# Performance work log

Measured on AMD Instinct MI355X. Metric: run time of the kernel, lower is better.

Reference implementation:

```python
import jax, jax.numpy as jnp
import numpy as np

# NSA hyperparams (match init_kwargs)
D_BLK = 64    # d: block stride
L_CMP = 64    # compression block length (== d -> non-overlapping blocks)
L_SLC = 64    # selection block length (== l_cmp == d -> P_slc = P_cmp)
BQ = 64       # block_size_q
TOPK = 16     # slc_top_k
WL, WR = 512, 0  # sliding window (left, right)


def _nsa_forward(q, k, v, w_k, b_k, w_v, b_v, w_gate, b_gate, seqlen):
    S, qh, dim = q.shape
    kv = k.shape[1]
    H = qh // kv
    b = S // seqlen          # number of equal-length packed sequences
    s = seqlen
    scale = dim ** -0.5
    f32 = jnp.float32

    # [b, s, kv, H, e]: q head g*H+h belongs to kv head g (repeat_interleave layout)
    q5 = q.reshape(b, s, kv, H, dim)
    k3 = k.reshape(b, s, kv, dim)
    v3 = v.reshape(b, s, kv, dim)

    # ---- block compression (extract_blocks + cmp_linear over block length) ----
    n_blk = s // D_BLK
    kb = k.reshape(b, n_blk, D_BLK, kv, dim)
    vb = v.reshape(b, n_blk, D_BLK, kv, dim)
    K_cmp = jnp.einsum('bntke,t->bnke', kb, w_k) + b_k[0]
    V_cmp = jnp.einsum('bntke,t->bnke', vb, w_v) + b_v[0]

    # ---- compressed attention (per sequence, fp32 softmax) ----
    sc = jnp.einsum('bqkhe,bnke->bkhqn', q5, K_cmp).astype(f32) * scale
    P = jax.nn.softmax(sc, axis=-1)
    out_cmp = jnp.einsum('bkhqn,bnke->bqkhe', P.astype(q.dtype), V_cmp)

    # ---- selection scores: pool P over q-blocks and GQA groups, then top-k ----
    nqb = s // BQ
    pooled = P.reshape(b, kv, H, nqb, BQ, n_blk).sum(axis=(2, 4))  # [b,kv,nqb,n_blk]
    idx = jax.lax.top_k(pooled, TOPK)[1]                            # [b,kv,nqb,TOPK]

    # gather selected K/V blocks (shared by all queries in a q-block / GQA group)
    kb2 = jnp.transpose(kb, (0, 3, 1, 2, 4))  # [b,kv,n_blk,l,e]
    vb2 = jnp.transpose(vb, (0, 3, 1, 2, 4))
    gather = jax.vmap(jax.vmap(lambda blocks, i: blocks[i]))
    K_sel = gather(kb2, idx)  # [b,kv,nqb,TOPK,l,e]
    V_sel = gather(vb2, idx)

    # ---- selected-block attention ----
    qblk = q5.reshape(b, nqb, BQ, kv, H, dim)
    sc2 = jnp.einsum('bnckhe,bkntle->bkhnctl', qblk, K_sel).astype(f32) * scale
    sc2 = sc2.reshape(b, kv, H, nqb, BQ, TOPK * L_SLC)
    P2 = jax.nn.softmax(sc2, axis=-1).astype(q.dtype)
    out_slc = jnp.einsum('bkhncm,bknme->bnckhe', P2,
                         V_sel.reshape(b, kv, nqb, TOPK * L_SLC, dim))
    out_slc = out_slc.reshape(b, s, kv, H, dim)

    # ---- sliding-window attention (window_size=(WL, WR), non-causal flag) ----
    sw = jnp.einsum('bikhe,bjke->bkhij', q5, k3).astype(f32) * scale
    i = jnp.arange(s)[:, None]
    j = jnp.arange(s)[None, :]
    valid = (j >= i - WL) & (j <= i + WR)
    sw = jnp.where(valid, sw, -jnp.inf)
    Pw = jax.nn.softmax(sw, axis=-1).astype(q.dtype)
    out_win = jnp.einsum('bkhij,bjke->bikhe', Pw, v3)

    # ---- gated fusion of the three branches ----
    gate = jax.nn.sigmoid(jnp.einsum('bqkhe,ec->bqkhc', q5, w_gate) + b_gate)
    out = (gate[..., 0:1] * out_cmp
           + gate[..., 1:2] * out_slc
           + gate[..., 2:3] * out_win)
    return out.reshape(S, qh, dim)


def setup_inputs() -> dict:
    key = jax.random.key(0)
    ks = jax.random.split(key, 9)
    S, qh, kvh, dim = 4096, 8, 2, 128
    inp = {
        'q': jax.random.normal(ks[0], (S, qh, dim), jnp.float32),
        'k': jax.random.normal(ks[1], (S, kvh, dim), jnp.float32),
        'v': jax.random.normal(ks[2], (S, kvh, dim), jnp.float32),
        'w_k': jax.random.normal(ks[3], (L_CMP,), jnp.float32) * (L_CMP ** -0.5),
        'b_k': jax.random.normal(ks[4], (1,), jnp.float32) * 0.02,
        'w_v': jax.random.normal(ks[5], (L_CMP,), jnp.float32) * (L_CMP ** -0.5),
        'b_v': jax.random.normal(ks[6], (1,), jnp.float32) * 0.02,
        'w_gate': jax.random.normal(ks[7], (dim, 3), jnp.float32) * (dim ** -0.5),
        'b_gate': jax.random.normal(ks[8], (3,), jnp.float32) * 0.02,
        'seqlen': 2048,
    }
    return inp


def reference(q, k, v, w_k, b_k, w_v, b_v, w_gate, b_gate, seqlen):
    return _nsa_forward(q, k, v, w_k, b_k, w_v, b_v, w_gate, b_gate, seqlen)
```

## Files before the change

kernel.cpp:

```cpp
#include <hip/hip_runtime.h>
#include <hip/hip_bf16.h>


#define SEQ   2048
#define NB    2
#define KV    2
#define NH    4
#define QH    8
#define DIM   128
#define NBLK  32
#define NQB   32
#define NTOP  16
#define SCALE 0.08838834764831845f
#define QSC   0.12751831795244785f
#define QS    36
#define RS    144
#define PLS   33
#define VP    72

typedef unsigned short ushort_t;
using bf16x8 = __attribute__((ext_vector_type(8))) short;
using f32x4  = __attribute__((ext_vector_type(4))) float;

__device__ __forceinline__ unsigned pkbf(float a, float b){
  union { __hip_bfloat162 h; unsigned u; } cv;
  cv.h = __float22bfloat162_rn(make_float2(a, b));
  return cv.u;
}

__device__ __forceinline__ void async16(ushort_t* l, const ushort_t* g){
  __builtin_amdgcn_global_load_lds(
      (const __attribute__((address_space(1))) unsigned int*)(size_t)g,
      (__attribute__((address_space(3))) unsigned int*)(size_t)l,
      16, 0, 0);
}

__global__ __launch_bounds__(256) void prep_k(
    const float* __restrict__ k, const float* __restrict__ v,
    const float* __restrict__ w_k, const float* __restrict__ b_k,
    const float* __restrict__ w_v, const float* __restrict__ b_v,
    ushort_t* __restrict__ Kb, ushort_t* __restrict__ VT,
    float* __restrict__ Kc, float* __restrict__ Vc)
{
  int blk = blockIdx.x;
  int db = blk & 1, rb = (blk >> 1) & 31, bbg = blk >> 6;
  int bb = bbg >> 1, g = bbg & 1;
  int tid = threadIdx.x;
  __shared__ ushort_t T[64*VP];
  __shared__ float wks[64], wvs[64];
  __shared__ float accK[16][64], accV[16][64];

  if (tid < 64){ wks[tid] = w_k[tid]; wvs[tid] = w_v[tid]; }
  __syncthreads();

  float4 sk = {0,0,0,0}, sv = {0,0,0,0};
  for (int jj = 0; jj < 4; ++jj){
    int i = tid + jj*256;
    int r = i >> 4, ds = i & 15;
    size_t src = ((size_t)(bb*SEQ + rb*64 + r)*KV + g)*DIM + db*64 + ds*4;
    float4 kx = *(const float4*)(k + src);
    float4 vx = *(const float4*)(v + src);
    uint2 kk; kk.x = pkbf(kx.x,kx.y); kk.y = pkbf(kx.z,kx.w);
    size_t rowb = ((size_t)bbg*SEQ + rb*64 + r)*DIM*2;
    int swz = (db*128 + ds*8) ^ ((r & 7) << 4);
    *(uint2*)((char*)Kb + rowb + swz) = kk;
    unsigned v01 = pkbf(vx.x,vx.y), v23 = pkbf(vx.z,vx.w);
    T[(ds*4+0)*VP + r] = (ushort_t)(v01 & 0xffffu);
    T[(ds*4+1)*VP + r] = (ushort_t)(v01 >> 16);
    T[(ds*4+2)*VP + r] = (ushort_t)(v23 & 0xffffu);
    T[(ds*4+3)*VP + r] = (ushort_t)(v23 >> 16);
    float a = wks[r], b = wvs[r];
    sk.x += a*kx.x; sk.y += a*kx.y; sk.z += a*kx.z; sk.w += a*kx.w;
    sv.x += b*vx.x; sv.y += b*vx.y; sv.z += b*vx.z; sv.w += b*vx.w;
  }
  *(float4*)&accK[tid>>4][(tid&15)*4] = sk;
  *(float4*)&accV[tid>>4][(tid&15)*4] = sv;
  __syncthreads();

  for (int jj = 0; jj < 4; ++jj){
    int i = tid + jj*256;
    int d = i >> 4, seg = i & 15;
    uint2 u = *(uint2*)&T[d*VP + seg*4];
    size_t rowb = ((size_t)bbg*DIM + db*64 + d)*SEQ*2;
    int swz = (seg*8) ^ ((d & 7) << 4);
    *(uint2*)((char*)VT + rowb + rb*128 + swz) = u;
  }

  size_t obase = ((size_t)(bbg*NBLK + rb))*DIM + db*64;
  if (tid < 64){
    float s = 0.f;
#pragma unroll
    for (int i = 0; i < 16; ++i) s += accK[i][tid];
    Kc[obase + tid] = s + b_k[0];
  } else if (tid < 128){
    int d = tid - 64;
    float s = 0.f;
#pragma unroll
    for (int i = 0; i < 16; ++i) s += accV[i][d];
    Vc[obase + d] = s + b_v[0];
  }
}

__global__ __launch_bounds__(256) void cmp_attn_k(
    const float* __restrict__ q, const float* __restrict__ Kc,
    const float* __restrict__ Vc,
    const float* __restrict__ w_gate, const float* __restrict__ b_gate,
    float* __restrict__ pooled_part, float* __restrict__ out)
{
  int blk = blockIdx.x;
  int h  = blk & 3;
  int qb = (blk >> 2) & (NQB-1);
  int g  = (blk >> 7) & 1;
  int bb = blk >> 8;
  int tid = threadIdx.x;
  int qi = tid >> 2, c = tid & 3;

  __shared__ float Ks[32*RS];
  __shared__ float Vs[32*RS];
  __shared__ float Pl[64*PLS];

  const float4* Ksrc = (const float4*)(Kc + (size_t)(bb*KV + g) * NBLK * DIM);
  const float4* Vsrc = (const float4*)(Vc + (size_t)(bb*KV + g) * NBLK * DIM);
  for (int i = tid; i < 1024; i += 256){
    int row = i >> 5, seg = i & 31;
    int dst = row*RS + (seg>>3)*QS + (seg&7)*4;
    ((float4*)(Ks+dst))[0] = Ksrc[i];
    ((float4*)(Vs+dst))[0] = Vsrc[i];
  }
  __syncthreads();

  int row = bb*SEQ + qb*64 + qi;
  const float* qptr = q + ((size_t)row*QH + g*NH + h)*DIM;

  float sc[8];
#pragma unroll
  for (int nn = 0; nn < 8; ++nn) sc[nn] = 0.f;
  float gp = 0.f;
  for (int qq = 0; qq < 4; ++qq){
    float qv[32];
    const float4* q4 = (const float4*)(qptr + qq*32);
#pragma unroll
    for (int j = 0; j < 8; ++j){
      float4 u = q4[j];
      qv[4*j+0]=u.x; qv[4*j+1]=u.y; qv[4*j+2]=u.z; qv[4*j+3]=u.w;
    }
#pragma unroll
    for (int d = 0; d < 32; ++d) gp += qv[d]*w_gate[(qq*32+d)*3 + 0];
#pragma unroll
    for (int nn = 0; nn < 8; ++nn){
      int n = nn*4 + c;
      const float4* kr = (const float4*)(Ks + n*RS + qq*QS);
      float p = 0.f;
#pragma unroll
      for (int j = 0; j < 8; ++j){
        float4 u = kr[j];
        p += qv[4*j+0]*u.x + qv[4*j+1]*u.y + qv[4*j+2]*u.z + qv[4*j+3]*u.w;
      }
      sc[nn] += p;
    }
  }
  float g0 = 1.f/(1.f + expf(-(gp + b_gate[0])));

#pragma unroll
  for (int nn = 0; nn < 8; ++nn) sc[nn] *= SCALE;
  float m = sc[0];
#pragma unroll
  for (int nn = 1; nn < 8; ++nn) m = fmaxf(m, sc[nn]);
  m = fmaxf(m, __shfl_xor(m, 1)); m = fmaxf(m, __shfl_xor(m, 2));
  float l = 0.f;
#pragma unroll
  for (int nn = 0; nn < 8; ++nn){ sc[nn] = expf(sc[nn]-m); l += sc[nn]; }
  l += __shfl_xor(l, 1); l += __shfl_xor(l, 2);
  float inv = 1.f/l;
#pragma unroll
  for (int nn = 0; nn < 8; ++nn) Pl[qi*PLS + nn*4 + c] = sc[nn]*inv;
  __syncthreads();

  if (tid < NBLK){
    float s = 0.f;
    for (int q2 = 0; q2 < 64; ++q2) s += Pl[q2*PLS + tid];
    pooled_part[(size_t)blk*NBLK + tid] = s;
  }

  float o[32];
#pragma unroll
  for (int d = 0; d < 32; ++d) o[d] = 0.f;
  for (int n = 0; n < NBLK; ++n){
    float pb = Pl[qi*PLS + n];
    const float4* vr = (const float4*)(Vs + n*RS + c*QS);
#pragma unroll
    for (int j = 0; j < 8; ++j){
      float4 u = vr[j];
      o[4*j+0] += pb*u.x; o[4*j+1] += pb*u.y;
      o[4*j+2] += pb*u.z; o[4*j+3] += pb*u.w;
    }
  }
  float* op = out + ((size_t)row*QH + g*NH + h)*DIM + c*32;
#pragma unroll
  for (int d = 0; d < 32; ++d) op[d] = g0*o[d];
}

__global__ __launch_bounds__(512, 2) void attn_k(
    const float* __restrict__ q, const ushort_t* __restrict__ Kb,
    const ushort_t* __restrict__ VT, const float* __restrict__ pp,
    const float* __restrict__ w_gate, const float* __restrict__ b_gate,
    float* __restrict__ slcbuf, float* __restrict__ out)
{
  int idx = blockIdx.x;
  int x = idx & 7, low = idx & 1, u = idx >> 3;
  int bbg = x >> 1;
  int j = u*2 + low;
  int role = j >> 5;
  int qb = j & 31;
  int bb = bbg >> 1, g = bbg & 1;

  int tid = threadIdx.x;
  int lane = tid & 63, w = tid >> 6;
  int quad = lane >> 4, l15 = lane & 15;
  int h = w & 3, qh2 = w >> 2;
  int xr = (l15 & 7) << 4;

  __shared__ ushort_t Ks[2][64*128];
  __shared__ ushort_t VTs[2][128*64];
  __shared__ ushort_t Ps[256*VP];
  __shared__ float gbuf[256];
  __shared__ int   idxs[NTOP];

  if (role == 0 && tid < 64){
    int n = lane;
    float val = -INFINITY;
    if (n < NBLK){
      const float* p0 = pp + ((size_t)((bb*KV+g)*NQB + qb)*NH)*NBLK + n;
      val = (p0[0] + p0[NBLK]) + (p0[2*NBLK] + p0[3*NBLK]);
    }
    for (int t = 0; t < NTOP; ++t){
      float bv = val; int bi = n;
      for (int mm = 1; mm < 32; mm <<= 1){
        float ov = __shfl_xor(bv, mm);
        int   oi = __shfl_xor(bi, mm);
        if (ov > bv || (ov == bv && oi < bi)){ bv = ov; bi = oi; }
      }
      if (lane == 0) idxs[t] = bi;
      if (n == bi) val = -INFINITY;
    }
  }

  const float* qrow0 = q + ((size_t)(bb*SEQ + qb*64 + qh2*32 + l15)*QH + g*NH + h)*DIM;
  const float* qrow1 = qrow0 + (size_t)16*QH*DIM;
  int gcol = 1 + role;
  bf16x8 qfrag0[4], qfrag1[4];
  float gp0 = 0.f, gp1 = 0.f;
#pragma unroll
  for (int kc = 0; kc < 4; ++kc){
    int d0 = kc*32 + quad*8;
    float4 a0 = *(const float4*)(qrow0 + d0);
    float4 a1 = *(const float4*)(qrow0 + d0 + 4);
    float4 b0 = *(const float4*)(qrow1 + d0);
    float4 b1 = *(const float4*)(qrow1 + d0 + 4);
    float qa[8] = {a0.x,a0.y,a0.z,a0.w,a1.x,a1.y,a1.z,a1.w};
    float qc[8] = {b0.x,b0.y,b0.z,b0.w,b1.x,b1.y,b1.z,b1.w};
#pragma unroll
    for (int jj = 0; jj < 8; ++jj){
      float wg = w_gate[(d0+jj)*3 + gcol];
      gp0 += qa[jj]*wg; gp1 += qc[jj]*wg;
    }
    union { unsigned uu[4]; bf16x8 v8; } t0, t1;
#pragma unroll
    for (int p2 = 0; p2 < 4; ++p2){
      t0.uu[p2] = pkbf(qa[2*p2]*QSC, qa[2*p2+1]*QSC);
      t1.uu[p2] = pkbf(qc[2*p2]*QSC, qc[2*p2+1]*QSC);
    }
    qfrag0[kc] = t0.v8; qfrag1[kc] = t1.v8;
  }
  gp0 += __shfl_xor(gp0,16); gp0 += __shfl_xor(gp0,32);
  gp1 += __shfl_xor(gp1,16); gp1 += __shfl_xor(gp1,32);
  if (quad == 0){
    gbuf[w*32 + l15]      = 1.f/(1.f + __expf(-(gp0 + b_gate[gcol])));
    gbuf[w*32 + 16 + l15] = 1.f/(1.f + __expf(-(gp1 + b_gate[gcol])));
  }
  __syncthreads();
  float gl0[4], gl1[4];
#pragma unroll
  for (int r = 0; r < 4; ++r){
    gl0[r] = gbuf[w*32 + quad*4 + r];
    gl1[r] = gbuf[w*32 + 16 + quad*4 + r];
  }

  const ushort_t* kbase  = Kb + (size_t)bbg*SEQ*DIM;
  const ushort_t* vtbase = VT + (size_t)bbg*DIM*SEQ;

  int kb0 = (qb >= 8) ? (qb - 8) : 0;
  int nph = (role == 0) ? NTOP : (qb - kb0 + 1);
  int qi0 = qh2*32 + l15, qi1 = qi0 + 16;

  float m10 = -INFINITY, l10 = 0.f, m11 = -INFINITY, l11 = 0.f;
  f32x4 oacc0[8], oacc1[8];
  const f32x4 zero4 = {0.f,0.f,0.f,0.f};
#pragma unroll
  for (int dt = 0; dt < 8; ++dt){ oacc0[dt] = zero4; oacc1[dt] = zero4; }

  auto stage = [&](int bufi, int kb_){
    const ushort_t* ksrc = kbase + (size_t)kb_*64*DIM;
#pragma unroll
    for (int jj = 0; jj < 2; ++jj)
      async16(&Ks[bufi][(jj*512 + w*64)*8], ksrc + (size_t)(tid + jj*512)*8);
    const ushort_t* vsrc = vtbase + kb_*64;
#pragma unroll
    for (int jj = 0; jj < 2; ++jj){
      int i = tid + jj*512;
      int d = i >> 3, sg = i & 7;
      async16(&VTs[bufi][(jj*512 + w*64)*8], vsrc + (size_t)d*SEQ + sg*8);
    }
  };

  stage(0, (role == 0) ? idxs[0] : kb0);

  for (int t = 0; t < nph; ++t){
    int cur = t & 1;
    int kb = (role == 0) ? idxs[t] : (kb0 + t);
    __syncthreads();
    if (t+1 < nph){
      int kbn = (role == 0) ? idxs[t+1] : (kb0 + t + 1);
      stage(cur ^ 1, kbn);
    }
    __builtin_amdgcn_sched_barrier(0);

    f32x4 sacc0[4], sacc1[4];
#pragma unroll
    for (int nt = 0; nt < 4; ++nt){ sacc0[nt] = zero4; sacc1[nt] = zero4; }
    __builtin_amdgcn_s_setprio(1);
#pragma unroll
    for (int kc = 0; kc < 4; ++kc){
#pragma unroll
      for (int nt = 0; nt < 4; ++nt){
        bf16x8 a = *(bf16x8*)((char*)&Ks[cur][0] + (nt*16 + l15)*256
                              + ((kc*64 + quad*16) ^ xr));
        sacc0[nt] = __builtin_amdgcn_mfma_f32_16x16x32_bf16(a, qfrag0[kc], sacc0[nt], 0, 0, 0);
        sacc1[nt] = __builtin_amdgcn_mfma_f32_16x16x32_bf16(a, qfrag1[kc], sacc1[nt], 0, 0, 0);
      }
    }
    __builtin_amdgcn_s_setprio(0);

    bool mlow  = (role == 1) && (kb == qb - 8);
    bool mhigh = (role == 1) && (kb == qb);
    bool domask = mlow | mhigh;

    auto softmax_qt = [&](f32x4* sc, float& m1r, float& l1r, int qi_l,
                          bool& skipped) -> float {
      float mx = -INFINITY;
      if (domask){
#pragma unroll
        for (int nt = 0; nt < 4; ++nt)
#pragma unroll
          for (int r = 0; r < 4; ++r){
            int key = nt*16 + quad*4 + r;
            float sv = sc[nt][r];
            bool valid = (!mlow || key >= qi_l) && (!mhigh || key <= qi_l);
            sv = valid ? sv : -INFINITY;
            sc[nt][r] = sv;
            mx = fmaxf(mx, sv);
          }
      } else {
#pragma unroll
        for (int nt = 0; nt < 4; ++nt)
#pragma unroll
          for (int r = 0; r < 4; ++r) mx = fmaxf(mx, sc[nt][r]);
      }
      mx = fmaxf(mx, __shfl_xor(mx, 16));
      mx = fmaxf(mx, __shfl_xor(mx, 32));
      float al = 1.f;
      skipped = __all(mx <= m1r + 8.f);
      if (!skipped){
        float mn = fmaxf(m1r, mx);
        al = exp2f(m1r - mn);
        m1r = mn;
      }
      float s0 = 0.f;
#pragma unroll
      for (int nt = 0; nt < 4; ++nt)
#pragma unroll
        for (int r = 0; r < 4; ++r){
          float pe = exp2f(sc[nt][r] - m1r);
          sc[nt][r] = pe;
          s0 += pe;
        }
      s0 += __shfl_xor(s0, 16);
      s0 += __shfl_xor(s0, 32);
      l1r = l1r*al + s0;
      return al;
    };
    bool sk0, sk1;
    float al0 = softmax_qt(sacc0, m10, l10, qi0, sk0);
    float al1 = softmax_qt(sacc1, m11, l11, qi1, sk1);

#pragma unroll
    for (int nt = 0; nt < 4; ++nt){
      uint2 p0, p1;
      p0.x = pkbf(sacc0[nt][0], sacc0[nt][1]);
      p0.y = pkbf(sacc0[nt][2], sacc0[nt][3]);
      p1.x = pkbf(sacc1[nt][0], sacc1[nt][1]);
      p1.y = pkbf(sacc1[nt][2], sacc1[nt][3]);
      *(uint2*)&Ps[(w*32 + l15)*VP + nt*16 + quad*4] = p0;
      *(uint2*)&Ps[(w*32 + 16 + l15)*VP + nt*16 + quad*4] = p1;
    }

    if (!sk0){
      float ar[4];
#pragma unroll
      for (int r = 0; r < 4; ++r) ar[r] = __shfl(al0, quad*4 + r);
#pragma unroll
      for (int dt = 0; dt < 8; ++dt)
#pragma unroll
        for (int r = 0; r < 4; ++r) oacc0[dt][r] *= ar[r];
    }
    if (!sk1){
      float ar[4];
#pragma unroll
      for (int r = 0; r < 4; ++r) ar[r] = __shfl(al1, quad*4 + r);
#pragma unroll
      for (int dt = 0; dt < 8; ++dt)
#pragma unroll
        for (int r = 0; r < 4; ++r) oacc1[dt][r] *= ar[r];
    }

#pragma unroll
    for (int kc2 = 0; kc2 < 2; ++kc2){
      bf16x8 pa0 = *(bf16x8*)&Ps[(w*32 + l15)*VP + kc2*32 + quad*8];
      bf16x8 pa1 = *(bf16x8*)&Ps[(w*32 + 16 + l15)*VP + kc2*32 + quad*8];
      __builtin_amdgcn_s_setprio(1);
#pragma unroll
      for (int dt = 0; dt < 8; ++dt){
        bf16x8 vb8 = *(bf16x8*)((char*)&VTs[cur][0] + (dt*16 + l15)*128
                                + ((kc2*64 + quad*16) ^ xr));
        oacc0[dt] = __builtin_amdgcn_mfma_f32_16x16x32_bf16(pa0, vb8, oacc0[dt], 0, 0, 0);
        oacc1[dt] = __builtin_amdgcn_mfma_f32_16x16x32_bf16(pa1, vb8, oacc1[dt], 0, 0, 0);
      }
      __builtin_amdgcn_s_setprio(0);
    }
  }

  float lr0[4], lr1[4];
#pragma unroll
  for (int r = 0; r < 4; ++r){
    lr0[r] = __shfl(l10, quad*4 + r);
    lr1[r] = __shfl(l11, quad*4 + r);
  }
#pragma unroll
  for (int r = 0; r < 4; ++r){
    float s20 = gl0[r] / lr0[r];
    float s21 = gl1[r] / lr1[r];
    size_t ob0 = ((size_t)(bb*SEQ + qb*64 + qh2*32 + quad*4 + r)*QH + g*NH + h)*DIM + l15;
    size_t ob1 = ob0 + (size_t)16*QH*DIM;
    if (role == 0){
      float* op0 = slcbuf + ob0;
      float* op1 = slcbuf + ob1;
#pragma unroll
      for (int dt = 0; dt < 8; ++dt){
        op0[dt*16] = s20 * oacc0[dt][r];
        op1[dt*16] = s21 * oacc1[dt][r];
      }
    } else {
      float* op0 = out + ob0;
      float* op1 = out + ob1;
#pragma unroll
      for (int dt = 0; dt < 8; ++dt){
        op0[dt*16] += s20 * oacc0[dt][r];
        op1[dt*16] += s21 * oacc1[dt][r];
      }
    }
  }
}

__global__ __launch_bounds__(256) void merge_k(const float* __restrict__ slcbuf,
                                               float* __restrict__ out){
  int i = blockIdx.x * 256 + threadIdx.x;
  float4 a = ((const float4*)slcbuf)[i];
  float4 b = ((float4*)out)[i];
  b.x += a.x; b.y += a.y; b.z += a.z; b.w += a.w;
  ((float4*)out)[i] = b;
}

extern "C" void kernel_launch(void* const* d_in, const int* in_sizes, int n_in,
                              void* d_out, int out_size, void* d_ws, size_t ws_size,
                              hipStream_t stream) {
  const float* q      = (const float*)d_in[0];
  const float* k      = (const float*)d_in[1];
  const float* v      = (const float*)d_in[2];
  const float* w_k    = (const float*)d_in[3];
  const float* b_k    = (const float*)d_in[4];
  const float* w_v    = (const float*)d_in[5];
  const float* b_v    = (const float*)d_in[6];
  const float* w_gate = (const float*)d_in[7];
  const float* b_gate = (const float*)d_in[8];
  float* out = (float*)d_out;

  float* ws     = (float*)d_ws;
  float* Kc     = ws;
  float* Vc     = ws + 16384;
  float* pp     = ws + 32768;
  float* slcbuf = ws + 49152;
  ushort_t* Kb  = (ushort_t*)(ws + 4243456);
  ushort_t* VT  = Kb + 1048576;

  prep_k    <<<256, 256, 0, stream>>>(k, v, w_k, b_k, w_v, b_v, Kb, VT, Kc, Vc);
  cmp_attn_k<<<NB*KV*NQB*NH, 256, 0, stream>>>(q, Kc, Vc, w_gate, b_gate, pp, out);
  attn_k    <<<256, 512, 0, stream>>>(q, Kb, VT, pp, w_gate, b_gate, slcbuf, out);
  merge_k   <<<4096, 256, 0, stream>>>(slcbuf, out);
}
```

Before: 178.6 us.

## Fuse compressed attention into selection kernel using split-bf16 MFMA

Removes the separate fp32 compressed-attention kernel and computes compressed scores, softmax, pooled selection scores and the compressed output inside the role-0 blocks of the main attention kernel. The products use MFMA with hi/lo bf16 splitting of Q, compressed K, V and P to keep close to fp32 accuracy, and top-k now reads pooled scores from shared memory instead of a global partial buffer. Role-1 blocks now write out directly rather than accumulating into it. This saves a kernel launch and the global traffic for pooled partials and the compressed output. In exchange, role-0 blocks carry extra serial work and more shared memory, which may reduce occupancy.

New measurement: 166.3 us. -6.8%, faster.

```diff
diff --git a/kernel.cpp b/kernel.cpp
--- a/kernel.cpp
+++ b/kernel.cpp
@@ -13,10 +13,8 @@
 #define NTOP  16
 #define SCALE 0.08838834764831845f
 #define QSC   0.12751831795244785f
-#define QS    36
-#define RS    144
-#define PLS   33
 #define VP    72
+#define VCS   40
 
 typedef unsigned short ushort_t;
 using bf16x8 = __attribute__((ext_vector_type(8))) short;
@@ -26,6 +24,15 @@
   union { __hip_bfloat162 h; unsigned u; } cv;
   cv.h = __float22bfloat162_rn(make_float2(a, b));
   return cv.u;
+}
+__device__ __forceinline__ ushort_t b16(float f){
+  union { float f; unsigned i; } x; x.f = f;
+  unsigned r = x.i + 0x7fffu + ((x.i >> 16) & 1u);
+  return (ushort_t)(r >> 16);
+}
+__device__ __forceinline__ float fb(ushort_t h){
+  union { unsigned i; float f; } x; x.i = ((unsigned)h) << 16;
+  return x.f;
 }
 
 __device__ __forceinline__ void async16(ushort_t* l, const ushort_t* g){
@@ -101,108 +108,10 @@
   }
 }
 
-__global__ __launch_bounds__(256) void cmp_attn_k(
-    const float* __restrict__ q, const float* __restrict__ Kc,
-    const float* __restrict__ Vc,
-    const float* __restrict__ w_gate, const float* __restrict__ b_gate,
-    float* __restrict__ pooled_part, float* __restrict__ out)
-{
-  int blk = blockIdx.x;
-  int h  = blk & 3;
-  int qb = (blk >> 2) & (NQB-1);
-  int g  = (blk >> 7) & 1;
-  int bb = blk >> 8;
-  int tid = threadIdx.x;
-  int qi = tid >> 2, c = tid & 3;
-
-  __shared__ float Ks[32*RS];
-  __shared__ float Vs[32*RS];
-  __shared__ float Pl[64*PLS];
-
-  const float4* Ksrc = (const float4*)(Kc + (size_t)(bb*KV + g) * NBLK * DIM);
-  const float4* Vsrc = (const float4*)(Vc + (size_t)(bb*KV + g) * NBLK * DIM);
-  for (int i = tid; i < 1024; i += 256){
-    int row = i >> 5, seg = i & 31;
-    int dst = row*RS + (seg>>3)*QS + (seg&7)*4;
-    ((float4*)(Ks+dst))[0] = Ksrc[i];
-    ((float4*)(Vs+dst))[0] = Vsrc[i];
-  }
-  __syncthreads();
-
-  int row = bb*SEQ + qb*64 + qi;
-  const float* qptr = q + ((size_t)row*QH + g*NH + h)*DIM;
-
-  float sc[8];
-#pragma unroll
-  for (int nn = 0; nn < 8; ++nn) sc[nn] = 0.f;
-  float gp = 0.f;
-  for (int qq = 0; qq < 4; ++qq){
-    float qv[32];
-    const float4* q4 = (const float4*)(qptr + qq*32);
-#pragma unroll
-    for (int j = 0; j < 8; ++j){
-      float4 u = q4[j];
-      qv[4*j+0]=u.x; qv[4*j+1]=u.y; qv[4*j+2]=u.z; qv[4*j+3]=u.w;
-    }
-#pragma unroll
-    for (int d = 0; d < 32; ++d) gp += qv[d]*w_gate[(qq*32+d)*3 + 0];
-#pragma unroll
-    for (int nn = 0; nn < 8; ++nn){
-      int n = nn*4 + c;
-      const float4* kr = (const float4*)(Ks + n*RS + qq*QS);
-      float p = 0.f;
-#pragma unroll
-      for (int j = 0; j < 8; ++j){
-        float4 u = kr[j];
-        p += qv[4*j+0]*u.x + qv[4*j+1]*u.y + qv[4*j+2]*u.z + qv[4*j+3]*u.w;
-      }
-      sc[nn] += p;
-    }
-  }
-  float g0 = 1.f/(1.f + expf(-(gp + b_gate[0])));
-
-#pragma unroll
-  for (int nn = 0; nn < 8; ++nn) sc[nn] *= SCALE;
-  float m = sc[0];
-#pragma unroll
-  for (int nn = 1; nn < 8; ++nn) m = fmaxf(m, sc[nn]);
-  m = fmaxf(m, __shfl_xor(m, 1)); m = fmaxf(m, __shfl_xor(m, 2));
-  float l = 0.f;
-#pragma unroll
-  for (int nn = 0; nn < 8; ++nn){ sc[nn] = expf(sc[nn]-m); l += sc[nn]; }
-  l += __shfl_xor(l, 1); l += __shfl_xor(l, 2);
-  float inv = 1.f/l;
-#pragma unroll
-  for (int nn = 0; nn < 8; ++nn) Pl[qi*PLS + nn*4 + c] = sc[nn]*inv;
-  __syncthreads();
-
-  if (tid < NBLK){
-    float s = 0.f;
-    for (int q2 = 0; q2 < 64; ++q2) s += Pl[q2*PLS + tid];
-    pooled_part[(size_t)blk*NBLK + tid] = s;
-  }
-
-  float o[32];
-#pragma unroll
-  for (int d = 0; d < 32; ++d) o[d] = 0.f;
-  for (int n = 0; n < NBLK; ++n){
-    float pb = Pl[qi*PLS + n];
-    const float4* vr = (const float4*)(Vs + n*RS + c*QS);
-#pragma unroll
-    for (int j = 0; j < 8; ++j){
-      float4 u = vr[j];
-      o[4*j+0] += pb*u.x; o[4*j+1] += pb*u.y;
-      o[4*j+2] += pb*u.z; o[4*j+3] += pb*u.w;
-    }
-  }
-  float* op = out + ((size_t)row*QH + g*NH + h)*DIM + c*32;
-#pragma unroll
-  for (int d = 0; d < 32; ++d) op[d] = g0*o[d];
-}
-
 __global__ __launch_bounds__(512, 2) void attn_k(
     const float* __restrict__ q, const ushort_t* __restrict__ Kb,
-    const ushort_t* __restrict__ VT, const float* __restrict__ pp,
+    const ushort_t* __restrict__ VT,
+    const float* __restrict__ Kc, const float* __restrict__ Vc,
     const float* __restrict__ w_gate, const float* __restrict__ b_gate,
     float* __restrict__ slcbuf, float* __restrict__ out)
 {
@@ -223,33 +132,48 @@
   __shared__ ushort_t Ks[2][64*128];
   __shared__ ushort_t VTs[2][128*64];
   __shared__ ushort_t Ps[256*VP];
+  __shared__ ushort_t VcTh[128*VCS];
+  __shared__ ushort_t VcTl[128*VCS];
+  __shared__ float pw[8][NBLK];
   __shared__ float gbuf[256];
   __shared__ int   idxs[NTOP];
 
-  if (role == 0 && tid < 64){
-    int n = lane;
-    float val = -INFINITY;
-    if (n < NBLK){
-      const float* p0 = pp + ((size_t)((bb*KV+g)*NQB + qb)*NH)*NBLK + n;
-      val = (p0[0] + p0[NBLK]) + (p0[2*NBLK] + p0[3*NBLK]);
-    }
-    for (int t = 0; t < NTOP; ++t){
-      float bv = val; int bi = n;
-      for (int mm = 1; mm < 32; mm <<= 1){
-        float ov = __shfl_xor(bv, mm);
-        int   oi = __shfl_xor(bi, mm);
-        if (ov > bv || (ov == bv && oi < bi)){ bv = ov; bi = oi; }
-      }
-      if (lane == 0) idxs[t] = bi;
-      if (n == bi) val = -INFINITY;
+  if (role == 0){
+    {
+      int key = tid >> 4, dq = tid & 15;
+      const float* kcs = Kc + ((size_t)bbg*NBLK + key)*DIM + dq*8;
+      float4 f0 = *(const float4*)kcs, f1 = *(const float4*)(kcs + 4);
+      float fe[8] = {f0.x,f0.y,f0.z,f0.w,f1.x,f1.y,f1.z,f1.w};
+      union { ushort_t u[8]; uint4 v; } hi, lo;
+#pragma unroll
+      for (int e = 0; e < 8; ++e){
+        ushort_t hh = b16(fe[e]);
+        hi.u[e] = hh; lo.u[e] = b16(fe[e] - fb(hh));
+      }
+      int off = (dq*16) ^ ((key & 7) << 4);
+      *(uint4*)((char*)&Ks[0][0] + key*256 + off) = hi.v;
+      *(uint4*)((char*)&Ks[0][0] + (key+32)*256 + off) = lo.v;
+    }
+    {
+      int d = tid & 127, kq = tid >> 7;
+      const float* vcs = Vc + (size_t)bbg*NBLK*DIM + d;
+      union { ushort_t u[8]; uint4 v; } hi, lo;
+#pragma unroll
+      for (int kk = 0; kk < 8; ++kk){
+        float f = vcs[(kq*8 + kk)*DIM];
+        ushort_t hh = b16(f);
+        hi.u[kk] = hh; lo.u[kk] = b16(f - fb(hh));
+      }
+      *(uint4*)&VcTh[d*VCS + kq*8] = hi.v;
+      *(uint4*)&VcTl[d*VCS + kq*8] = lo.v;
     }
   }
 
   const float* qrow0 = q + ((size_t)(bb*SEQ + qb*64 + qh2*32 + l15)*QH + g*NH + h)*DIM;
   const float* qrow1 = qrow0 + (size_t)16*QH*DIM;
   int gcol = 1 + role;
-  bf16x8 qfrag0[4], qfrag1[4];
-  float gp0 = 0.f, gp1 = 0.f;
+  bf16x8 qfrag0[4], qfrag1[4], qlo0[4], qlo1[4];
+  float gp0 = 0.f, gp1 = 0.f, gc0 = 0.f, gc1 = 0.f;
 #pragma unroll
   for (int kc = 0; kc < 4; ++kc){
     int d0 = kc*32 + quad*8;
@@ -264,13 +188,31 @@
       float wg = w_gate[(d0+jj)*3 + gcol];
       gp0 += qa[jj]*wg; gp1 += qc[jj]*wg;
     }
-    union { unsigned uu[4]; bf16x8 v8; } t0, t1;
-#pragma unroll
-    for (int p2 = 0; p2 < 4; ++p2){
-      t0.uu[p2] = pkbf(qa[2*p2]*QSC, qa[2*p2+1]*QSC);
-      t1.uu[p2] = pkbf(qc[2*p2]*QSC, qc[2*p2+1]*QSC);
-    }
-    qfrag0[kc] = t0.v8; qfrag1[kc] = t1.v8;
+    if (role == 0){
+#pragma unroll
+      for (int jj = 0; jj < 8; ++jj){
+        float w0 = w_gate[(d0+jj)*3];
+        gc0 += qa[jj]*w0; gc1 += qc[jj]*w0;
+      }
+      union { ushort_t u[8]; bf16x8 v; } h0, l0, h1, l1;
+#pragma unroll
+      for (int e = 0; e < 8; ++e){
+        float s0f = qa[e]*QSC; ushort_t hh0 = b16(s0f);
+        h0.u[e] = hh0; l0.u[e] = b16(s0f - fb(hh0));
+        float s1f = qc[e]*QSC; ushort_t hh1 = b16(s1f);
+        h1.u[e] = hh1; l1.u[e] = b16(s1f - fb(hh1));
+      }
+      qfrag0[kc] = h0.v; qlo0[kc] = l0.v;
+      qfrag1[kc] = h1.v; qlo1[kc] = l1.v;
+    } else {
+      union { unsigned uu[4]; bf16x8 v8; } t0, t1;
+#pragma unroll
+      for (int p2 = 0; p2 < 4; ++p2){
+        t0.uu[p2] = pkbf(qa[2*p2]*QSC, qa[2*p2+1]*QSC);
+        t1.uu[p2] = pkbf(qc[2*p2]*QSC, qc[2*p2+1]*QSC);
+      }
+      qfrag0[kc] = t0.v8; qfrag1[kc] = t1.v8;
+    }
   }
   gp0 += __shfl_xor(gp0,16); gp0 += __shfl_xor(gp0,32);
   gp1 += __shfl_xor(gp1,16); gp1 += __shfl_xor(gp1,32);
@@ -278,6 +220,13 @@
     gbuf[w*32 + l15]      = 1.f/(1.f + __expf(-(gp0 + b_gate[gcol])));
     gbuf[w*32 + 16 + l15] = 1.f/(1.f + __expf(-(gp1 + b_gate[gcol])));
   }
+  float g0c0 = 0.f, g0c1 = 0.f;
+  if (role == 0){
+    gc0 += __shfl_xor(gc0,16); gc0 += __shfl_xor(gc0,32);
+    gc1 += __shfl_xor(gc1,16); gc1 += __shfl_xor(gc1,32);
+    g0c0 = 1.f/(1.f + __expf(-(gc0 + b_gate[0])));
+    g0c1 = 1.f/(1.f + __expf(-(gc1 + b_gate[0])));
+  }
   __syncthreads();
   float gl0[4], gl1[4];
 #pragma unroll
@@ -286,6 +235,85 @@
     gl1[r] = gbuf[w*32 + 16 + quad*4 + r];
   }
 
+  const f32x4 zero4 = {0.f,0.f,0.f,0.f};
+  f32x4 cp0[2], cp1[2];
+  cp0[0] = zero4; cp0[1] = zero4; cp1[0] = zero4; cp1[1] = zero4;
+
+  if (role == 0){
+    f32x4 c0[2], c1[2];
+    c0[0]=zero4; c0[1]=zero4; c1[0]=zero4; c1[1]=zero4;
+#pragma unroll
+    for (int kc = 0; kc < 4; ++kc){
+#pragma unroll
+      for (int nt = 0; nt < 2; ++nt){
+        bf16x8 ah = *(bf16x8*)((char*)&Ks[0][0] + (nt*16 + l15)*256
+                               + ((kc*64 + quad*16) ^ xr));
+        bf16x8 al = *(bf16x8*)((char*)&Ks[0][0] + (nt*16 + l15 + 32)*256
+                               + ((kc*64 + quad*16) ^ xr));
+        c0[nt] = __builtin_amdgcn_mfma_f32_16x16x32_bf16(ah, qfrag0[kc], c0[nt], 0, 0, 0);
+        c0[nt] = __builtin_amdgcn_mfma_f32_16x16x32_bf16(ah, qlo0[kc],   c0[nt], 0, 0, 0);
+        c0[nt] = __builtin_amdgcn_mfma_f32_16x16x32_bf16(al, qfrag0[kc], c0[nt], 0, 0, 0);
+        c1[nt] = __builtin_amdgcn_mfma_f32_16x16x32_bf16(ah, qfrag1[kc], c1[nt], 0, 0, 0);
+        c1[nt] = __builtin_amdgcn_mfma_f32_16x16x32_bf16(ah, qlo1[kc],   c1[nt], 0, 0, 0);
+        c1[nt] = __builtin_amdgcn_mfma_f32_16x16x32_bf16(al, qfrag1[kc], c1[nt], 0, 0, 0);
+      }
+    }
+    float mx0 = -INFINITY, mx1 = -INFINITY;
+#pragma unroll
+    for (int nt = 0; nt < 2; ++nt)
+#pragma unroll
+      for (int r = 0; r < 4; ++r){
+        mx0 = fmaxf(mx0, c0[nt][r]); mx1 = fmaxf(mx1, c1[nt][r]);
+      }
+    mx0 = fmaxf(mx0, __shfl_xor(mx0,16)); mx0 = fmaxf(mx0, __shfl_xor(mx0,32));
+    mx1 = fmaxf(mx1, __shfl_xor(mx1,16)); mx1 = fmaxf(mx1, __shfl_xor(mx1,32));
+    float s0 = 0.f, s1 = 0.f;
+#pragma unroll
+    for (int nt = 0; nt < 2; ++nt)
+#pragma unroll
+      for (int r = 0; r < 4; ++r){
+        float p0v = exp2f(c0[nt][r] - mx0); c0[nt][r] = p0v; s0 += p0v;
+        float p1v = exp2f(c1[nt][r] - mx1); c1[nt][r] = p1v; s1 += p1v;
+      }
+    s0 += __shfl_xor(s0,16); s0 += __shfl_xor(s0,32);
+    s1 += __shfl_xor(s1,16); s1 += __shfl_xor(s1,32);
+    float ip0 = 1.f/s0, ip1 = 1.f/s1;
+    float ig0 = g0c0*ip0, ig1 = g0c1*ip1;
+#pragma unroll
+    for (int nt = 0; nt < 2; ++nt)
+#pragma unroll
+      for (int r = 0; r < 4; ++r){
+        cp0[nt][r] = c0[nt][r]*ig0;
+        cp1[nt][r] = c1[nt][r]*ig1;
+        float t = c0[nt][r]*ip0 + c1[nt][r]*ip1;
+        t += __shfl_xor(t,1); t += __shfl_xor(t,2);
+        t += __shfl_xor(t,4); t += __shfl_xor(t,8);
+        if (l15 == 0) pw[w][nt*16 + quad*4 + r] = t;
+      }
+    __syncthreads();
+    if (tid < 64){
+      int n = lane;
+      float val = -INFINITY;
+      if (n < NBLK){
+        float sm = 0.f;
+#pragma unroll
+        for (int w2 = 0; w2 < 8; ++w2) sm += pw[w2][n];
+        val = sm;
+      }
+      for (int t = 0; t < NTOP; ++t){
+        float bv = val; int bi = n;
+        for (int mm = 1; mm < 32; mm <<= 1){
+          float ov = __shfl_xor(bv, mm);
+          int   oi = __shfl_xor(bi, mm);
+          if (ov > bv || (ov == bv && oi < bi)){ bv = ov; bi = oi; }
+        }
+        if (lane == 0) idxs[t] = bi;
+        if (n == bi) val = -INFINITY;
+      }
+    }
+    __syncthreads();
+  }
+
   const ushort_t* kbase  = Kb + (size_t)bbg*SEQ*DIM;
   const ushort_t* vtbase = VT + (size_t)bbg*DIM*SEQ;
 
@@ -295,7 +323,6 @@
 
   float m10 = -INFINITY, l10 = 0.f, m11 = -INFINITY, l11 = 0.f;
   f32x4 oacc0[8], oacc1[8];
-  const f32x4 zero4 = {0.f,0.f,0.f,0.f};
 #pragma unroll
   for (int dt = 0; dt < 8; ++dt){ oacc0[dt] = zero4; oacc1[dt] = zero4; }
 
@@ -345,7 +372,7 @@
     bool mhigh = (role == 1) && (kb == qb);
     bool domask = mlow | mhigh;
 
-    auto softmax_qt = [&](f32x4* sc, float& m1r, float& l1r, int qi_l,
+    auto softmax_qt = [&](f32x4* sc2, float& m1r, float& l1r, int qi_l,
                           bool& skipped) -> float {
       float mx = -INFINITY;
       if (domask){
@@ -354,17 +381,17 @@
 #pragma unroll
           for (int r = 0; r < 4; ++r){
             int key = nt*16 + quad*4 + r;
-            float sv = sc[nt][r];
+            float sv = sc2[nt][r];
             bool valid = (!mlow || key >= qi_l) && (!mhigh || key <= qi_l);
             sv = valid ? sv : -INFINITY;
-            sc[nt][r] = sv;
+            sc2[nt][r] = sv;
             mx = fmaxf(mx, sv);
           }
       } else {
 #pragma unroll
         for (int nt = 0; nt < 4; ++nt)
 #pragma unroll
-          for (int r = 0; r < 4; ++r) mx = fmaxf(mx, sc[nt][r]);
+          for (int r = 0; r < 4; ++r) mx = fmaxf(mx, sc2[nt][r]);
       }
       mx = fmaxf(mx, __shfl_xor(mx, 16));
       mx = fmaxf(mx, __shfl_xor(mx, 32));
@@ -380,8 +407,8 @@
       for (int nt = 0; nt < 4; ++nt)
 #pragma unroll
         for (int r = 0; r < 4; ++r){
-          float pe = exp2f(sc[nt][r] - m1r);
-          sc[nt][r] = pe;
+          float pe = exp2f(sc2[nt][r] - m1r);
+          sc2[nt][r] = pe;
           s0 += pe;
         }
       s0 += __shfl_xor(s0, 16);
@@ -445,27 +472,69 @@
     lr0[r] = __shfl(l10, quad*4 + r);
     lr1[r] = __shfl(l11, quad*4 + r);
   }
-#pragma unroll
-  for (int r = 0; r < 4; ++r){
-    float s20 = gl0[r] / lr0[r];
-    float s21 = gl1[r] / lr1[r];
-    size_t ob0 = ((size_t)(bb*SEQ + qb*64 + qh2*32 + quad*4 + r)*QH + g*NH + h)*DIM + l15;
-    size_t ob1 = ob0 + (size_t)16*QH*DIM;
-    if (role == 0){
+  if (role == 0){
+    float a0[4], a1[4];
+#pragma unroll
+    for (int r = 0; r < 4; ++r){ a0[r] = gl0[r]/lr0[r]; a1[r] = gl1[r]/lr1[r]; }
+#pragma unroll
+    for (int dt = 0; dt < 8; ++dt)
+#pragma unroll
+      for (int r = 0; r < 4; ++r){ oacc0[dt][r] *= a0[r]; oacc1[dt][r] *= a1[r]; }
+#pragma unroll
+    for (int nt = 0; nt < 2; ++nt){
+      union { ushort_t u[4]; uint2 v; } h0, l0, h1, l1;
+#pragma unroll
+      for (int r = 0; r < 4; ++r){
+        ushort_t hh0 = b16(cp0[nt][r]);
+        h0.u[r] = hh0; l0.u[r] = b16(cp0[nt][r] - fb(hh0));
+        ushort_t hh1 = b16(cp1[nt][r]);
+        h1.u[r] = hh1; l1.u[r] = b16(cp1[nt][r] - fb(hh1));
+      }
+      *(uint2*)&Ps[(w*32 + l15)*VP + nt*16 + quad*4]      = h0.v;
+      *(uint2*)&Ps[(w*32 + l15)*VP + 32 + nt*16 + quad*4] = l0.v;
+      *(uint2*)&Ps[(w*32 + 16 + l15)*VP + nt*16 + quad*4]      = h1.v;
+      *(uint2*)&Ps[(w*32 + 16 + l15)*VP + 32 + nt*16 + quad*4] = l1.v;
+    }
+    bf16x8 pah0 = *(bf16x8*)&Ps[(w*32 + l15)*VP + quad*8];
+    bf16x8 pal0 = *(bf16x8*)&Ps[(w*32 + l15)*VP + 32 + quad*8];
+    bf16x8 pah1 = *(bf16x8*)&Ps[(w*32 + 16 + l15)*VP + quad*8];
+    bf16x8 pal1 = *(bf16x8*)&Ps[(w*32 + 16 + l15)*VP + 32 + quad*8];
+#pragma unroll
+    for (int dt = 0; dt < 8; ++dt){
+      bf16x8 vbh = *(bf16x8*)&VcTh[(dt*16 + l15)*VCS + quad*8];
+      bf16x8 vbl = *(bf16x8*)&VcTl[(dt*16 + l15)*VCS + quad*8];
+      oacc0[dt] = __builtin_amdgcn_mfma_f32_16x16x32_bf16(pah0, vbh, oacc0[dt], 0, 0, 0);
+      oacc0[dt] = __builtin_amdgcn_mfma_f32_16x16x32_bf16(pah0, vbl, oacc0[dt], 0, 0, 0);
+      oacc0[dt] = __builtin_amdgcn_mfma_f32_16x16x32_bf16(pal0, vbh, oacc0[dt], 0, 0, 0);
+      oacc1[dt] = __builtin_amdgcn_mfma_f32_16x16x32_bf16(pah1, vbh, oacc1[dt], 0, 0, 0);
+      oacc1[dt] = __builtin_amdgcn_mfma_f32_16x16x32_bf16(pah1, vbl, oacc1[dt], 0, 0, 0);
+      oacc1[dt] = __builtin_amdgcn_mfma_f32_16x16x32_bf16(pal1, vbh, oacc1[dt], 0, 0, 0);
+    }
+#pragma unroll
+    for (int r = 0; r < 4; ++r){
+      size_t ob0 = ((size_t)(bb*SEQ + qb*64 + qh2*32 + quad*4 + r)*QH + g*NH + h)*DIM + l15;
+      size_t ob1 = ob0 + (size_t)16*QH*DIM;
       float* op0 = slcbuf + ob0;
       float* op1 = slcbuf + ob1;
+#pragma unroll
+      for (int dt = 0; dt < 8; ++dt){
+        op0[dt*16] = oacc0[dt][r];
+        op1[dt*16] = oacc1[dt][r];
+      }
+    }
+  } else {
+#pragma unroll
+    for (int r = 0; r < 4; ++r){
+      float s20 = gl0[r] / lr0[r];
+      float s21 = gl1[r] / lr1[r];
+      size_t ob0 = ((size_t)(bb*SEQ + qb*64 + qh2*32 + quad*4 + r)*QH + g*NH + h)*DIM + l15;
+      size_t ob1 = ob0 + (size_t)16*QH*DIM;
+      float* op0 = out + ob0;
+      float* op1 = out + ob1;
 #pragma unroll
       for (int dt = 0; dt < 8; ++dt){
         op0[dt*16] = s20 * oacc0[dt][r];
         op1[dt*16] = s21 * oacc1[dt][r];
-      }
-    } else {
-      float* op0 = out + ob0;
-      float* op1 = out + ob1;
-#pragma unroll
-      for (int dt = 0; dt < 8; ++dt){
-        op0[dt*16] += s20 * oacc0[dt][r];
-        op1[dt*16] += s21 * oacc1[dt][r];
       }
     }
   }
@@ -497,13 +566,11 @@
   float* ws     = (float*)d_ws;
   float* Kc     = ws;
   float* Vc     = ws + 16384;
-  float* pp     = ws + 32768;
   float* slcbuf = ws + 49152;
   ushort_t* Kb  = (ushort_t*)(ws + 4243456);
   ushort_t* VT  = Kb + 1048576;
 
-  prep_k    <<<256, 256, 0, stream>>>(k, v, w_k, b_k, w_v, b_v, Kb, VT, Kc, Vc);
-  cmp_attn_k<<<NB*KV*NQB*NH, 256, 0, stream>>>(q, Kc, Vc, w_gate, b_gate, pp, out);
-  attn_k    <<<256, 512, 0, stream>>>(q, Kb, VT, pp, w_gate, b_gate, slcbuf, out);
-  merge_k   <<<4096, 256, 0, stream>>>(slcbuf, out);
-}
+  prep_k <<<256, 256, 0, stream>>>(k, v, w_k, b_k, w_v, b_v, Kb, VT, Kc, Vc);
+  attn_k <<<256, 512, 0, stream>>>(q, Kb, VT, Kc, Vc, w_gate, b_gate, slcbuf, out);
+  merge_k<<<4096, 256, 0, stream>>>(slcbuf, out);
+}
```
